# Kernel tuning notes

Hardware: AMD Instinct MI355X
Metric: run time of the kernel (lower is better)

The kernel has to match this reference:

```python
import jax, jax.numpy as jnp
import numpy as np
import itertools

WS = (4, 4, 4, 2, 2)          # window size per dim
SS = (2, 2, 2, 1, 1)          # shift size per dim
B, D, H, W, U, V, C = 1, 16, 16, 8, 8, 8, 128
HEADS = 4
HD = C // HEADS
N = WS[0] * WS[1] * WS[2] * WS[3] * WS[4]   # 256 tokens per window


def _partition(x):
    # (b, D,H,W,U,V, c) -> (b*nW, N, c)
    b, c = x.shape[0], x.shape[-1]
    x = x.reshape(b, D // WS[0], WS[0], H // WS[1], WS[1], W // WS[2], WS[2],
                  U // WS[3], WS[3], V // WS[4], WS[4], c)
    x = x.transpose(0, 1, 3, 5, 7, 9, 2, 4, 6, 8, 10, 11)
    return x.reshape(-1, N, c)


def _reverse(win, b):
    # (b*nW, N, c) -> (b, D,H,W,U,V, c)
    c = win.shape[-1]
    x = win.reshape(b, D // WS[0], H // WS[1], W // WS[2], U // WS[3], V // WS[4],
                    WS[0], WS[1], WS[2], WS[3], WS[4], c)
    x = x.transpose(0, 1, 6, 2, 7, 3, 8, 4, 9, 5, 10, 11)
    return x.reshape(b, D, H, W, U, V, c)


def _ln(x, w, b, eps=1e-5):
    mu = jnp.mean(x, -1, keepdims=True)
    xc = x - mu
    var = jnp.mean(xc * xc, -1, keepdims=True)
    return xc * jax.lax.rsqrt(var + eps) * w + b


def _compute_mask():
    # 5D generalization of Swin's compute_mask: region labels then pairwise diff
    img = np.zeros((1, D, H, W, U, V, 1), np.float32)
    slcs = [[slice(0, -w), slice(-w, -s), slice(-s, None)] for w, s in zip(WS, SS)]
    cnt = 0
    for idx in itertools.product(*slcs):
        img[(slice(None),) + idx] = cnt
        cnt += 1
    mw = np.asarray(_partition(jnp.asarray(img))).squeeze(-1)  # (nW, N)
    diff = mw[:, None, :] - mw[:, :, None]
    return jnp.asarray(np.where(diff != 0, -1e9, 0.0).astype(np.float32))


def setup_inputs() -> dict:
    key = jax.random.key(0)
    ks = jax.random.split(key, 6)
    s = 0.02
    return {
        "x": jax.random.normal(ks[0], (B, D, H, W, U, V, C), jnp.float32),
        "mask": _compute_mask(),  # (512, 256, 256)
        "qkv_w": jax.random.normal(ks[1], (3 * C, C), jnp.float32) * s,
        "qkv_b": jnp.zeros((3 * C,), jnp.float32),
        "proj_w": jax.random.normal(ks[2], (C, C), jnp.float32) * s,
        "proj_b": jnp.zeros((C,), jnp.float32),
        "norm1_w": jnp.ones((C,), jnp.float32),
        "norm1_b": jnp.zeros((C,), jnp.float32),
        "norm2_w": jnp.ones((C,), jnp.float32),
        "norm2_b": jnp.zeros((C,), jnp.float32),
        "fc1_w": jax.random.normal(ks[3], (4 * C, C), jnp.float32) * s,
        "fc1_b": jnp.zeros((4 * C,), jnp.float32),
        "fc2_w": jax.random.normal(ks[4], (C, 4 * C), jnp.float32) * s,
        "fc2_b": jnp.zeros((C,), jnp.float32),
    }


def reference(x, mask, qkv_w, qkv_b, proj_w, proj_b, norm1_w, norm1_b,
              norm2_w, norm2_b, fc1_w, fc1_b, fc2_w, fc2_b):
    shortcut = x
    h = _ln(x, norm1_w, norm1_b)
    # cyclic shift
    h = jnp.roll(h, shift=tuple(-s for s in SS), axis=(1, 2, 3, 4, 5))
    win = _partition(h)                                # (nW, N, C)
    nw = win.shape[0]
    qkv = win @ qkv_w.T + qkv_b                        # (nW, N, 3C)
    qkv = qkv.reshape(nw, N, 3, HEADS, HD).transpose(2, 0, 3, 1, 4)
    q, k, v = qkv[0] * (HD ** -0.5), qkv[1], qkv[2]    # (nW, heads, N, hd)
    logits = jnp.einsum('bhnc,bhmc->bhnm', q, k) + mask[:, None]
    attn = jax.nn.softmax(logits, axis=-1)
    o = jnp.einsum('bhnm,bhmc->bhnc', attn, v)
    o = o.transpose(0, 2, 1, 3).reshape(nw, N, C)
    o = o @ proj_w.T + proj_b
    h = _reverse(o, B)
    # reverse cyclic shift
    h = jnp.roll(h, shift=SS, axis=(1, 2, 3, 4, 5))
    x = shortcut + h
    m = _ln(x, norm2_w, norm2_b)
    m = jax.nn.gelu(m @ fc1_w.T + fc1_b, approximate=False)
    m = m @ fc2_w.T + fc2_b
    return x + m
```

## Files before the change

kernel.cpp:

```cpp
#include <hip/hip_runtime.h>
#include <math.h>

typedef short bf16x8 __attribute__((ext_vector_type(8)));
typedef float f32x4 __attribute__((ext_vector_type(4)));
typedef unsigned short ushort_t;
typedef unsigned int uint_t;

__device__ __forceinline__ float bf2f(ushort_t h) { return __uint_as_float(((uint_t)h) << 16); }
__device__ __forceinline__ ushort_t f2bf(float f) {
    uint_t u = __float_as_uint(f);
    u += 0x7fffu + ((u >> 16) & 1u);
    return (ushort_t)(u >> 16);
}
__device__ __forceinline__ float bflo(uint_t u) { return __uint_as_float(u << 16); }
__device__ __forceinline__ float bfhi(uint_t u) { return __uint_as_float(u & 0xffff0000u); }

__device__ __forceinline__ bool probe_f32(const void* ones) {
    return ((const ushort_t*)ones)[0] == 0;
}

__device__ __forceinline__ void load8f(const void* p, size_t idx, bool f32, float* o) {
    if (f32) {
        const float4* q = (const float4*)((const float*)p + idx);
        float4 a = q[0], b = q[1];
        o[0] = a.x; o[1] = a.y; o[2] = a.z; o[3] = a.w;
        o[4] = b.x; o[5] = b.y; o[6] = b.z; o[7] = b.w;
    } else {
        uint4 u = *(const uint4*)((const ushort_t*)p + idx);
        o[0] = bflo(u.x); o[1] = bfhi(u.x); o[2] = bflo(u.y); o[3] = bfhi(u.y);
        o[4] = bflo(u.z); o[5] = bfhi(u.z); o[6] = bflo(u.w); o[7] = bfhi(u.w);
    }
}

__device__ __forceinline__ float load1(const void* p, size_t i, bool f32) {
    return f32 ? ((const float*)p)[i] : bf2f(((const ushort_t*)p)[i]);
}
__device__ __forceinline__ void store1(void* p, size_t i, bool f32, float v) {
    if (f32) ((float*)p)[i] = v;
    else ((ushort_t*)p)[i] = f2bf(v);
}

__device__ __forceinline__ float gelu_f(float x) {
    float ax = fabsf(x) * 0.70710678118654752f;
    float t = __builtin_amdgcn_rcpf(1.f + 0.3275911f * ax);
    float p = t * (0.254829592f +
              t * (-0.284496736f +
              t * (1.421413741f +
              t * (-1.453152027f +
              t * 1.061405429f))));
    float e = __expf(-ax * ax);
    float erfv = 1.f - p * e;
    float phi = 0.5f * (1.f + copysignf(erfv, x));
    return x * phi;
}

__device__ __forceinline__ void token_g(int t, int g[5]) {
    int n = t & 255, w = t >> 8;
    int wv = w & 3, wu = (w >> 2) & 3, ww = (w >> 4) & 1, wh = (w >> 5) & 3, wd = (w >> 7) & 3;
    int iv = n & 1, iu = (n >> 1) & 1, iw = (n >> 2) & 3, ih = (n >> 4) & 3, id = (n >> 6) & 3;
    g[0] = wd * 4 + id;
    g[1] = wh * 4 + ih;
    g[2] = ww * 4 + iw;
    g[3] = wu * 2 + iu;
    g[4] = wv * 2 + iv;
}

__device__ __forceinline__ int token_shiftpix(int t) {
    int g[5];
    token_g(t, g);
    int d = (g[0] + 2) & 15, h = (g[1] + 2) & 15, w = (g[2] + 2) & 7;
    int u = (g[3] + 1) & 7, v = (g[4] + 1) & 7;
    return ((((d * 16 + h) * 8 + w) * 8 + u) * 8 + v);
}

__device__ __forceinline__ int token_label(int t) {
    int g[5];
    token_g(t, g);
    int r0 = g[0] < 12 ? 0 : (g[0] < 14 ? 1 : 2);
    int r1 = g[1] < 12 ? 0 : (g[1] < 14 ? 1 : 2);
    int r2 = g[2] < 4 ? 0 : (g[2] < 6 ? 1 : 2);
    int r3 = g[3] < 6 ? 0 : (g[3] < 7 ? 1 : 2);
    int r4 = g[4] < 6 ? 0 : (g[4] < 7 ? 1 : 2);
    return (((r0 * 3 + r1) * 3 + r2) * 3 + r3) * 3 + r4;
}

#define MFMA16(a, b, c) __builtin_amdgcn_mfma_f32_16x16x32_bf16(a, b, c, 0, 0, 0)

#define QW_N 49152
#define PW_N 16384
#define W1_N 65536
#define W2_N 65536

__global__ __launch_bounds__(256) void k_prep(const void* __restrict__ qw,
                                              const void* __restrict__ pw,
                                              const void* __restrict__ w1,
                                              const void* __restrict__ w2,
                                              const void* __restrict__ probe,
                                              ushort_t* __restrict__ out) {
    const bool f32 = probe_f32(probe);
    size_t e = ((size_t)blockIdx.x * 256 + threadIdx.x) * 8;
    float v[8];
    size_t dst;
    if (e < QW_N) {
        load8f(qw, e, f32, v);
        dst = e;
    } else if (e < QW_N + PW_N) {
        load8f(pw, e - QW_N, f32, v);
        dst = e;
    } else if (e < QW_N + PW_N + W1_N) {
        size_t off = e - (QW_N + PW_N);
        load8f(w1, off, f32, v);
        int n = (int)(off >> 7), k = (int)(off & 127);
        int chunk = ((n >> 4) * 4 + (k >> 5)) * 64 + ((k >> 3) & 3) * 16 + (n & 15);
        dst = (size_t)(QW_N + PW_N) + (size_t)chunk * 8;
    } else {
        size_t off = e - (QW_N + PW_N + W1_N);
        load8f(w2, off, f32, v);
        int n = (int)(off >> 9), k = (int)(off & 511);
        int chunk = ((n >> 4) * 16 + (k >> 5)) * 64 + ((k >> 3) & 3) * 16 + (n & 15);
        dst = (size_t)(QW_N + PW_N + W1_N) + (size_t)chunk * 8;
    }
    union { uint4 q; ushort_t u[8]; } pk;
#pragma unroll
    for (int j = 0; j < 8; j++) pk.u[j] = f2bf(v[j]);
    *reinterpret_cast<uint4*>(out + dst) = pk.q;
}

__global__ __launch_bounds__(256) void k_qkv(const void* __restrict__ x,
                                             const void* __restrict__ n1w,
                                             const void* __restrict__ n1b,
                                             const ushort_t* __restrict__ qwb,
                                             const void* __restrict__ qb,
                                             ushort_t* __restrict__ qT,
                                             ushort_t* __restrict__ kT,
                                             ushort_t* __restrict__ vF) {
    __shared__ __align__(16) ushort_t sA[128][136];
    __shared__ __align__(16) ushort_t sB[128][136];
    const bool f32 = probe_f32(n1w);
    const int tid = threadIdx.x;
    const int ct = blockIdx.x;
    const int rt = blockIdx.y;

    {
        int i = tid >> 1, half = tid & 1;
        int t = rt * 128 + i;
        int pix = token_shiftpix(t);
        float v[64];
        float s1 = 0.f, s2 = 0.f;
#pragma unroll
        for (int j = 0; j < 8; j++) {
            load8f(x, (size_t)pix * 128 + half * 64 + j * 8, f32, &v[j * 8]);
#pragma unroll
            for (int e = 0; e < 8; e++) { float f = v[j * 8 + e]; s1 += f; s2 += f * f; }
        }
        s1 += __shfl_xor(s1, 1);
        s2 += __shfl_xor(s2, 1);
        float mean = s1 * (1.f / 128.f);
        float var = s2 * (1.f / 128.f) - mean * mean;
        float rstd = rsqrtf(fmaxf(var, 0.f) + 1e-5f);
#pragma unroll
        for (int j = 0; j < 64; j++) {
            int c = half * 64 + j;
            float nv = (v[j] - mean) * rstd * load1(n1w, c, f32) + load1(n1b, c, f32);
            sA[i][c] = f2bf(nv);
        }
    }
    {
        int i = tid >> 1, half = tid & 1;
        const uint4* wr = (const uint4*)(qwb + (size_t)(ct * 128 + i) * 128 + half * 64);
#pragma unroll
        for (int j = 0; j < 8; j++)
            *reinterpret_cast<uint4*>(&sB[i][half * 64 + j * 8]) = wr[j];
    }
    __syncthreads();

    const int lane = tid & 63, wvid = tid >> 6;
    const int quad = lane >> 4, l16 = lane & 15;
    const int mbase = (wvid >> 1) * 64, nbase = (wvid & 1) * 64;
    f32x4 acc[4][4];
#pragma unroll
    for (int a = 0; a < 4; a++)
#pragma unroll
        for (int b = 0; b < 4; b++) acc[a][b] = (f32x4){0.f, 0.f, 0.f, 0.f};

#pragma unroll
    for (int k0 = 0; k0 < 128; k0 += 32) {
        bf16x8 af[4], bg[4];
#pragma unroll
        for (int mi = 0; mi < 4; mi++)
            af[mi] = *reinterpret_cast<const bf16x8*>(&sA[mbase + mi * 16 + l16][k0 + quad * 8]);
#pragma unroll
        for (int ni = 0; ni < 4; ni++)
            bg[ni] = *reinterpret_cast<const bf16x8*>(&sB[nbase + ni * 16 + l16][k0 + quad * 8]);
#pragma unroll
        for (int mi = 0; mi < 4; mi++)
#pragma unroll
            for (int ni = 0; ni < 4; ni++) acc[mi][ni] = MFMA16(af[mi], bg[ni], acc[mi][ni]);
    }
    const int wbase4 = (rt >> 1) * 4;
    const int nadd = (rt & 1) * 128;
#pragma unroll
    for (int ni = 0; ni < 4; ni++) {
        int col = nbase + ni * 16 + l16;
        float bias = load1(qb, ct * 128 + col, f32);
        int h = col >> 5, d = col & 31;
        size_t whbase = (size_t)(wbase4 + h) * 8192;
#pragma unroll
        for (int mi = 0; mi < 4; mi++) {
#pragma unroll
            for (int r = 0; r < 4; r++) {
                int row = mbase + mi * 16 + quad * 4 + r;
                int n = nadd + row;
                float val = acc[mi][ni][r] + bias;
                if (ct == 0) {
                    qT[whbase + (size_t)n * 32 + d] = f2bf(val);
                } else if (ct == 1) {
                    kT[whbase + (size_t)n * 32 + d] = f2bf(val);
                } else {
                    size_t idx = whbase + (size_t)(n >> 5) * 1024 + (size_t)(d >> 4) * 512 +
                                 (size_t)((n >> 3) & 3) * 128 + (size_t)(d & 15) * 8 + (n & 7);
                    vF[idx] = f2bf(val);
                }
            }
        }
    }
}

__global__ __launch_bounds__(256) void k_attn(const ushort_t* __restrict__ qT,
                                              const ushort_t* __restrict__ kT,
                                              const ushort_t* __restrict__ vF,
                                              ushort_t* __restrict__ o) {
    __shared__ __align__(16) ushort_t sS[64][264];
    __shared__ unsigned char sLab[256];
    const int tid = threadIdx.x;
    const int rb = blockIdx.x, hh = blockIdx.y, w = blockIdx.z;
    const size_t whbase = (size_t)(w * 4 + hh) * 8192;

    sLab[tid] = (unsigned char)token_label(w * 256 + tid);
    __syncthreads();

    const int lane = tid & 63, wvid = tid >> 6, quad = lane >> 4, l16 = lane & 15;
    const int r0 = wvid * 16;

    bf16x8 aq = *reinterpret_cast<const bf16x8*>(
        qT + whbase + (size_t)(rb * 64 + r0 + l16) * 32 + quad * 8);

    f32x4 s[16];
    int myLab[4];
#pragma unroll
    for (int r = 0; r < 4; r++) myLab[r] = sLab[rb * 64 + r0 + quad * 4 + r];
#pragma unroll
    for (int ni = 0; ni < 16; ni++) {
        bf16x8 bk = *reinterpret_cast<const bf16x8*>(
            kT + whbase + (size_t)(ni * 16 + l16) * 32 + quad * 8);
        f32x4 c = (f32x4){0.f, 0.f, 0.f, 0.f};
        c = MFMA16(aq, bk, c);
        int klab = sLab[ni * 16 + l16];
#pragma unroll
        for (int r = 0; r < 4; r++)
            s[ni][r] = (klab == myLab[r]) ? c[r] * 0.17677669529663687f : -1.0e30f;
    }
    float mx[4], sm[4], inv[4];
#pragma unroll
    for (int r = 0; r < 4; r++) {
        float m2 = s[0][r];
#pragma unroll
        for (int ni = 1; ni < 16; ni++) m2 = fmaxf(m2, s[ni][r]);
        m2 = fmaxf(m2, __shfl_xor(m2, 1));
        m2 = fmaxf(m2, __shfl_xor(m2, 2));
        m2 = fmaxf(m2, __shfl_xor(m2, 4));
        m2 = fmaxf(m2, __shfl_xor(m2, 8));
        mx[r] = m2;
    }
#pragma unroll
    for (int r = 0; r < 4; r++) sm[r] = 0.f;
#pragma unroll
    for (int ni = 0; ni < 16; ni++) {
#pragma unroll
        for (int r = 0; r < 4; r++) {
            float p = __expf(s[ni][r] - mx[r]);
            s[ni][r] = p;
            sm[r] += p;
        }
    }
#pragma unroll
    for (int r = 0; r < 4; r++) {
        float t2 = sm[r];
        t2 += __shfl_xor(t2, 1);
        t2 += __shfl_xor(t2, 2);
        t2 += __shfl_xor(t2, 4);
        t2 += __shfl_xor(t2, 8);
        inv[r] = 1.f / t2;
    }
#pragma unroll
    for (int ni = 0; ni < 16; ni++) {
#pragma unroll
        for (int r = 0; r < 4; r++)
            sS[r0 + quad * 4 + r][ni * 16 + l16] = f2bf(s[ni][r]);
    }
    __syncthreads();

    f32x4 oacc[2];
    oacc[0] = (f32x4){0.f, 0.f, 0.f, 0.f};
    oacc[1] = (f32x4){0.f, 0.f, 0.f, 0.f};
#pragma unroll
    for (int kt = 0; kt < 8; kt++) {
        bf16x8 ap = *reinterpret_cast<const bf16x8*>(&sS[r0 + l16][kt * 32 + quad * 8]);
#pragma unroll
        for (int t2 = 0; t2 < 2; t2++) {
            bf16x8 bv = *reinterpret_cast<const bf16x8*>(
                vF + whbase + (size_t)((kt * 2 + t2) * 64 + lane) * 8);
            oacc[t2] = MFMA16(ap, bv, oacc[t2]);
        }
    }
#pragma unroll
    for (int t2 = 0; t2 < 2; t2++) {
#pragma unroll
        for (int r = 0; r < 4; r++) {
            int row = r0 + quad * 4 + r;
            int tok = w * 256 + rb * 64 + row;
            o[(size_t)tok * 128 + hh * 32 + t2 * 16 + l16] = f2bf(oacc[t2][r] * inv[r]);
        }
    }
}

__global__ __launch_bounds__(256) void k_proj(const ushort_t* __restrict__ o,
                                              const ushort_t* __restrict__ pwb,
                                              const void* __restrict__ pb,
                                              const void* __restrict__ x,
                                              const void* __restrict__ n1w,
                                              float* __restrict__ x2) {
    __shared__ __align__(16) ushort_t sA[128][136];
    __shared__ __align__(16) ushort_t sB[128][136];
    __shared__ int sPix[128];
    const bool f32 = probe_f32(n1w);
    const int tid = threadIdx.x;
    const int rt = blockIdx.x;

    if (tid < 128) sPix[tid] = token_shiftpix(rt * 128 + tid);
    {
        int i = tid >> 1, half = tid & 1;
        const uint4* src = (const uint4*)(o + (size_t)(rt * 128 + i) * 128 + half * 64);
        const uint4* wsrc = (const uint4*)(pwb + (size_t)i * 128 + half * 64);
#pragma unroll
        for (int j = 0; j < 8; j++) {
            *reinterpret_cast<uint4*>(&sA[i][half * 64 + j * 8]) = src[j];
            *reinterpret_cast<uint4*>(&sB[i][half * 64 + j * 8]) = wsrc[j];
        }
    }
    __syncthreads();

    const int lane = tid & 63, wvid = tid >> 6;
    const int quad = lane >> 4, l16 = lane & 15;
    const int mbase = (wvid >> 1) * 64, nbase = (wvid & 1) * 64;
    f32x4 acc[4][4];
#pragma unroll
    for (int a = 0; a < 4; a++)
#pragma unroll
        for (int b = 0; b < 4; b++) acc[a][b] = (f32x4){0.f, 0.f, 0.f, 0.f};

#pragma unroll
    for (int k0 = 0; k0 < 128; k0 += 32) {
        bf16x8 af[4], bg[4];
#pragma unroll
        for (int mi = 0; mi < 4; mi++)
            af[mi] = *reinterpret_cast<const bf16x8*>(&sA[mbase + mi * 16 + l16][k0 + quad * 8]);
#pragma unroll
        for (int ni = 0; ni < 4; ni++)
            bg[ni] = *reinterpret_cast<const bf16x8*>(&sB[nbase + ni * 16 + l16][k0 + quad * 8]);
#pragma unroll
        for (int mi = 0; mi < 4; mi++)
#pragma unroll
            for (int ni = 0; ni < 4; ni++) acc[mi][ni] = MFMA16(af[mi], bg[ni], acc[mi][ni]);
    }
#pragma unroll
    for (int ni = 0; ni < 4; ni++) {
        int col = nbase + ni * 16 + l16;
        float bias = load1(pb, col, f32);
#pragma unroll
        for (int mi = 0; mi < 4; mi++) {
#pragma unroll
            for (int r = 0; r < 4; r++) {
                int row = mbase + mi * 16 + quad * 4 + r;
                int pix = sPix[row];
                size_t idx = (size_t)pix * 128 + col;
                x2[idx] = acc[mi][ni][r] + bias + load1(x, idx, f32);
            }
        }
    }
}

__global__ __launch_bounds__(256) void k_mlp(const float* __restrict__ x2,
                                             const void* __restrict__ n2w,
                                             const void* __restrict__ n2b,
                                             const ushort_t* __restrict__ w1f,
                                             const void* __restrict__ b1,
                                             const ushort_t* __restrict__ w2f,
                                             const void* __restrict__ b2,
                                             void* __restrict__ out) {
    __shared__ __align__(16) ushort_t sH[32][516];
    ushort_t (*sM)[136] = reinterpret_cast<ushort_t (*)[136]>(&sH[0][0]);
    const bool f32 = probe_f32(n2w);
    const int tid = threadIdx.x;
    const int t0 = blockIdx.x * 32;

    {
        int i = tid >> 3, oct = tid & 7;
        const float* row = x2 + (size_t)(t0 + i) * 128 + oct * 16;
        float v[16];
        float s1 = 0.f, s2 = 0.f;
#pragma unroll
        for (int j = 0; j < 4; j++) {
            float4 f = ((const float4*)row)[j];
            v[j * 4 + 0] = f.x; v[j * 4 + 1] = f.y; v[j * 4 + 2] = f.z; v[j * 4 + 3] = f.w;
            s1 += f.x + f.y + f.z + f.w;
            s2 += f.x * f.x + f.y * f.y + f.z * f.z + f.w * f.w;
        }
        s1 += __shfl_xor(s1, 1); s2 += __shfl_xor(s2, 1);
        s1 += __shfl_xor(s1, 2); s2 += __shfl_xor(s2, 2);
        s1 += __shfl_xor(s1, 4); s2 += __shfl_xor(s2, 4);
        float mean = s1 * (1.f / 128.f);
        float rstd = rsqrtf(fmaxf(s2 * (1.f / 128.f) - mean * mean, 0.f) + 1e-5f);
#pragma unroll
        for (int j = 0; j < 16; j++) {
            int c = oct * 16 + j;
            sM[i][c] = f2bf((v[j] - mean) * rstd * load1(n2w, c, f32) + load1(n2b, c, f32));
        }
    }
    __syncthreads();

    const int lane = tid & 63, wvid = tid >> 6, quad = lane >> 4, l16 = lane & 15;

    bf16x8 af[2][4];
#pragma unroll
    for (int mi = 0; mi < 2; mi++)
#pragma unroll
        for (int k4 = 0; k4 < 4; k4++)
            af[mi][k4] = *reinterpret_cast<const bf16x8*>(&sM[mi * 16 + l16][k4 * 32 + quad * 8]);
    __syncthreads();

    {
        const int cb = wvid * 128;
        bf16x8 wf[4], wn[4];
#pragma unroll
        for (int k4 = 0; k4 < 4; k4++)
            wf[k4] = *reinterpret_cast<const bf16x8*>(
                w1f + (size_t)(((wvid * 8) * 4 + k4) * 64 + lane) * 8);
#pragma unroll
        for (int ni = 0; ni < 8; ni++) {
            if (ni < 7) {
#pragma unroll
                for (int k4 = 0; k4 < 4; k4++)
                    wn[k4] = *reinterpret_cast<const bf16x8*>(
                        w1f + (size_t)(((wvid * 8 + ni + 1) * 4 + k4) * 64 + lane) * 8);
            }
            f32x4 a0 = (f32x4){0.f, 0.f, 0.f, 0.f};
            f32x4 a1 = (f32x4){0.f, 0.f, 0.f, 0.f};
#pragma unroll
            for (int k4 = 0; k4 < 4; k4++) {
                a0 = MFMA16(af[0][k4], wf[k4], a0);
                a1 = MFMA16(af[1][k4], wf[k4], a1);
            }
            int col = cb + ni * 16 + l16;
            float bias = load1(b1, col, f32);
#pragma unroll
            for (int r = 0; r < 4; r++) {
                sH[quad * 4 + r][col] = f2bf(gelu_f(a0[r] + bias));
                sH[16 + quad * 4 + r][col] = f2bf(gelu_f(a1[r] + bias));
            }
#pragma unroll
            for (int k4 = 0; k4 < 4; k4++) wf[k4] = wn[k4];
        }
    }
    __syncthreads();
    {
        const int cb = wvid * 32;
        float res[2][2][4];
#pragma unroll
        for (int mi = 0; mi < 2; mi++)
#pragma unroll
            for (int ni = 0; ni < 2; ni++)
#pragma unroll
                for (int r = 0; r < 4; r++)
                    res[mi][ni][r] = x2[(size_t)(t0 + mi * 16 + quad * 4 + r) * 128 + cb + ni * 16 + l16];
        f32x4 acc[2][2];
#pragma unroll
        for (int mi = 0; mi < 2; mi++)
#pragma unroll
            for (int ni = 0; ni < 2; ni++) acc[mi][ni] = (f32x4){0.f, 0.f, 0.f, 0.f};
        bf16x8 wf[2], wn[2];
#pragma unroll
        for (int ni = 0; ni < 2; ni++)
            wf[ni] = *reinterpret_cast<const bf16x8*>(
                w2f + (size_t)(((wvid * 2 + ni) * 16) * 64 + lane) * 8);
#pragma unroll
        for (int k0 = 0; k0 < 16; k0++) {
            if (k0 < 15) {
#pragma unroll
                for (int ni = 0; ni < 2; ni++)
                    wn[ni] = *reinterpret_cast<const bf16x8*>(
                        w2f + (size_t)(((wvid * 2 + ni) * 16 + k0 + 1) * 64 + lane) * 8);
            }
            bf16x8 a0 = *reinterpret_cast<const bf16x8*>(&sH[l16][k0 * 32 + quad * 8]);
            bf16x8 a1 = *reinterpret_cast<const bf16x8*>(&sH[16 + l16][k0 * 32 + quad * 8]);
            acc[0][0] = MFMA16(a0, wf[0], acc[0][0]);
            acc[1][0] = MFMA16(a1, wf[0], acc[1][0]);
            acc[0][1] = MFMA16(a0, wf[1], acc[0][1]);
            acc[1][1] = MFMA16(a1, wf[1], acc[1][1]);
            wf[0] = wn[0];
            wf[1] = wn[1];
        }
#pragma unroll
        for (int ni = 0; ni < 2; ni++) {
            int col = cb + ni * 16 + l16;
            float bias = load1(b2, col, f32);
#pragma unroll
            for (int mi = 0; mi < 2; mi++) {
#pragma unroll
                for (int r = 0; r < 4; r++) {
                    int row = mi * 16 + quad * 4 + r;
                    size_t idx = (size_t)(t0 + row) * 128 + col;
                    store1(out, idx, f32, acc[mi][ni][r] + bias + res[mi][ni][r]);
                }
            }
        }
    }
}

extern "C" void kernel_launch(void* const* d_in, const int* in_sizes, int n_in,
                              void* d_out, int out_size, void* d_ws, size_t ws_size,
                              hipStream_t stream) {
    (void)in_sizes; (void)n_in; (void)out_size; (void)ws_size;
    const void* x   = d_in[0];
    const void* qw  = d_in[2];
    const void* qb  = d_in[3];
    const void* pw  = d_in[4];
    const void* pb  = d_in[5];
    const void* n1w = d_in[6];
    const void* n1b = d_in[7];
    const void* n2w = d_in[8];
    const void* n2b = d_in[9];
    const void* w1  = d_in[10];
    const void* b1  = d_in[11];
    const void* w2  = d_in[12];
    const void* b2  = d_in[13];

    ushort_t* qT  = (ushort_t*)d_ws;
    ushort_t* kT  = (ushort_t*)((char*)d_ws + 33554432);
    ushort_t* vF  = (ushort_t*)((char*)d_ws + 67108864);
    ushort_t* ob  = (ushort_t*)((char*)d_ws + 100663296);
    float* x2     = (float*)d_ws;
    ushort_t* wts = (ushort_t*)((char*)d_ws + 134217728);
    ushort_t* qwb = wts;
    ushort_t* pwb = wts + QW_N;
    ushort_t* w1f = wts + QW_N + PW_N;
    ushort_t* w2f = wts + QW_N + PW_N + W1_N;

    hipLaunchKernelGGL(k_prep, dim3(96), dim3(256), 0, stream, qw, pw, w1, w2, n1w, wts);
    hipLaunchKernelGGL(k_qkv, dim3(3, 1024), dim3(256), 0, stream, x, n1w, n1b, qwb, qb, qT, kT, vF);
    hipLaunchKernelGGL(k_attn, dim3(4, 4, 512), dim3(256), 0, stream, qT, kT, vF, ob);
    hipLaunchKernelGGL(k_proj, dim3(1024), dim3(256), 0, stream, ob, pwb, pb, x, n1w, x2);
    hipLaunchKernelGGL(k_mlp, dim3(4096), dim3(256), 0, stream, x2, n2w, n2b, w1f, b1, w2f, b2, d_out);
}
```

Before: 560.6 us.

## Merge QKV column tiles per block and read MFMA-fragment weights from global

The QKV kernel now handles all three Q/K/V column tiles in one block, looping over them, so the LayerNorm of x is done once per row tile instead of three times. The prep kernel reorders the qkv and proj weights into an MFMA fragment-major layout, so the B operand is loaded straight from global/L2 with coalesced 16-byte loads and no shared-memory staging. Halving shared memory plus launch_bounds(256,4) is meant to raise occupancy. The trade-off is that weight reads now depend on cache hits from global memory, and each block does more serial work over a grid three times smaller.

```diff
diff --git a/kernel.cpp b/kernel.cpp
--- a/kernel.cpp
+++ b/kernel.cpp
@@ -103,10 +103,15 @@
     size_t dst;
     if (e < QW_N) {
         load8f(qw, e, f32, v);
-        dst = e;
+        int n = (int)(e >> 7), k = (int)(e & 127);
+        int chunk = ((n >> 4) * 4 + (k >> 5)) * 64 + ((k >> 3) & 3) * 16 + (n & 15);
+        dst = (size_t)chunk * 8;
     } else if (e < QW_N + PW_N) {
-        load8f(pw, e - QW_N, f32, v);
-        dst = e;
+        size_t off = e - QW_N;
+        load8f(pw, off, f32, v);
+        int n = (int)(off >> 7), k = (int)(off & 127);
+        int chunk = ((n >> 4) * 4 + (k >> 5)) * 64 + ((k >> 3) & 3) * 16 + (n & 15);
+        dst = (size_t)QW_N + (size_t)chunk * 8;
     } else if (e < QW_N + PW_N + W1_N) {
         size_t off = e - (QW_N + PW_N);
         load8f(w1, off, f32, v);
@@ -126,20 +131,18 @@
     *reinterpret_cast<uint4*>(out + dst) = pk.q;
 }
 
-__global__ __launch_bounds__(256) void k_qkv(const void* __restrict__ x,
-                                             const void* __restrict__ n1w,
-                                             const void* __restrict__ n1b,
-                                             const ushort_t* __restrict__ qwb,
-                                             const void* __restrict__ qb,
-                                             ushort_t* __restrict__ qT,
-                                             ushort_t* __restrict__ kT,
-                                             ushort_t* __restrict__ vF) {
+__global__ __launch_bounds__(256, 4) void k_qkv(const void* __restrict__ x,
+                                                const void* __restrict__ n1w,
+                                                const void* __restrict__ n1b,
+                                                const ushort_t* __restrict__ qwF,
+                                                const void* __restrict__ qb,
+                                                ushort_t* __restrict__ qT,
+                                                ushort_t* __restrict__ kT,
+                                                ushort_t* __restrict__ vF) {
     __shared__ __align__(16) ushort_t sA[128][136];
-    __shared__ __align__(16) ushort_t sB[128][136];
     const bool f32 = probe_f32(n1w);
     const int tid = threadIdx.x;
-    const int ct = blockIdx.x;
-    const int rt = blockIdx.y;
+    const int rt = blockIdx.x;
 
     {
         int i = tid >> 1, half = tid & 1;
@@ -159,67 +162,70 @@
         float var = s2 * (1.f / 128.f) - mean * mean;
         float rstd = rsqrtf(fmaxf(var, 0.f) + 1e-5f);
 #pragma unroll
-        for (int j = 0; j < 64; j++) {
-            int c = half * 64 + j;
-            float nv = (v[j] - mean) * rstd * load1(n1w, c, f32) + load1(n1b, c, f32);
-            sA[i][c] = f2bf(nv);
-        }
-    }
-    {
-        int i = tid >> 1, half = tid & 1;
-        const uint4* wr = (const uint4*)(qwb + (size_t)(ct * 128 + i) * 128 + half * 64);
-#pragma unroll
-        for (int j = 0; j < 8; j++)
-            *reinterpret_cast<uint4*>(&sB[i][half * 64 + j * 8]) = wr[j];
-    }
-    __syncthreads();
-
-    const int lane = tid & 63, wvid = tid >> 6;
-    const int quad = lane >> 4, l16 = lane & 15;
+        for (int j = 0; j < 8; j++) {
+            float wv[8], bv[8];
+            load8f(n1w, half * 64 + j * 8, f32, wv);
+            load8f(n1b, half * 64 + j * 8, f32, bv);
+            union { uint4 q; ushort_t u[8]; } pk;
+#pragma unroll
+            for (int e = 0; e < 8; e++)
+                pk.u[e] = f2bf((v[j * 8 + e] - mean) * rstd * wv[e] + bv[e]);
+            *reinterpret_cast<uint4*>(&sA[i][half * 64 + j * 8]) = pk.q;
+        }
+    }
+    __syncthreads();
+
+    const int lane = tid & 63, wvid = tid >> 6, quad = lane >> 4, l16 = lane & 15;
     const int mbase = (wvid >> 1) * 64, nbase = (wvid & 1) * 64;
-    f32x4 acc[4][4];
-#pragma unroll
-    for (int a = 0; a < 4; a++)
-#pragma unroll
-        for (int b = 0; b < 4; b++) acc[a][b] = (f32x4){0.f, 0.f, 0.f, 0.f};
-
-#pragma unroll
-    for (int k0 = 0; k0 < 128; k0 += 32) {
-        bf16x8 af[4], bg[4];
-#pragma unroll
-        for (int mi = 0; mi < 4; mi++)
-            af[mi] = *reinterpret_cast<const bf16x8*>(&sA[mbase + mi * 16 + l16][k0 + quad * 8]);
-#pragma unroll
-        for (int ni = 0; ni < 4; ni++)
-            bg[ni] = *reinterpret_cast<const bf16x8*>(&sB[nbase + ni * 16 + l16][k0 + quad * 8]);
-#pragma unroll
-        for (int mi = 0; mi < 4; mi++)
-#pragma unroll
-            for (int ni = 0; ni < 4; ni++) acc[mi][ni] = MFMA16(af[mi], bg[ni], acc[mi][ni]);
-    }
+    const int tnb = (wvid & 1) * 4;
     const int wbase4 = (rt >> 1) * 4;
     const int nadd = (rt & 1) * 128;
-#pragma unroll
-    for (int ni = 0; ni < 4; ni++) {
-        int col = nbase + ni * 16 + l16;
-        float bias = load1(qb, ct * 128 + col, f32);
-        int h = col >> 5, d = col & 31;
-        size_t whbase = (size_t)(wbase4 + h) * 8192;
-#pragma unroll
-        for (int mi = 0; mi < 4; mi++) {
-#pragma unroll
-            for (int r = 0; r < 4; r++) {
-                int row = mbase + mi * 16 + quad * 4 + r;
-                int n = nadd + row;
-                float val = acc[mi][ni][r] + bias;
-                if (ct == 0) {
-                    qT[whbase + (size_t)n * 32 + d] = f2bf(val);
-                } else if (ct == 1) {
-                    kT[whbase + (size_t)n * 32 + d] = f2bf(val);
-                } else {
-                    size_t idx = whbase + (size_t)(n >> 5) * 1024 + (size_t)(d >> 4) * 512 +
-                                 (size_t)((n >> 3) & 3) * 128 + (size_t)(d & 15) * 8 + (n & 7);
-                    vF[idx] = f2bf(val);
+
+#pragma unroll 1
+    for (int ct = 0; ct < 3; ct++) {
+        f32x4 acc[4][4];
+#pragma unroll
+        for (int a = 0; a < 4; a++)
+#pragma unroll
+            for (int b = 0; b < 4; b++) acc[a][b] = (f32x4){0.f, 0.f, 0.f, 0.f};
+
+#pragma unroll
+        for (int k4 = 0; k4 < 4; k4++) {
+            bf16x8 af[4], bg[4];
+#pragma unroll
+            for (int mi = 0; mi < 4; mi++)
+                af[mi] = *reinterpret_cast<const bf16x8*>(&sA[mbase + mi * 16 + l16][k4 * 32 + quad * 8]);
+#pragma unroll
+            for (int ni = 0; ni < 4; ni++)
+                bg[ni] = *reinterpret_cast<const bf16x8*>(
+                    qwF + (size_t)(((ct * 8 + tnb + ni) * 4 + k4) * 64 + lane) * 8);
+#pragma unroll
+            for (int mi = 0; mi < 4; mi++)
+#pragma unroll
+                for (int ni = 0; ni < 4; ni++) acc[mi][ni] = MFMA16(af[mi], bg[ni], acc[mi][ni]);
+        }
+#pragma unroll
+        for (int ni = 0; ni < 4; ni++) {
+            int col = nbase + ni * 16 + l16;
+            float bias = load1(qb, ct * 128 + col, f32);
+            int h = col >> 5, d = col & 31;
+            size_t whbase = (size_t)(wbase4 + h) * 8192;
+#pragma unroll
+            for (int mi = 0; mi < 4; mi++) {
+#pragma unroll
+                for (int r = 0; r < 4; r++) {
+                    int row = mbase + mi * 16 + quad * 4 + r;
+                    int n = nadd + row;
+                    float val = acc[mi][ni][r] + bias;
+                    if (ct == 0) {
+                        qT[whbase + (size_t)n * 32 + d] = f2bf(val);
+                    } else if (ct == 1) {
+                        kT[whbase + (size_t)n * 32 + d] = f2bf(val);
+                    } else {
+                        size_t idx = whbase + (size_t)(n >> 5) * 1024 + (size_t)(d >> 4) * 512 +
+                                     (size_t)((n >> 3) & 3) * 128 + (size_t)(d & 15) * 8 + (n & 7);
+                        vF[idx] = f2bf(val);
+                    }
                 }
             }
         }
@@ -324,14 +330,13 @@
     }
 }
 
-__global__ __launch_bounds__(256) void k_proj(const ushort_t* __restrict__ o,
-                                              const ushort_t* __restrict__ pwb,
-                                              const void* __restrict__ pb,
-                                              const void* __restrict__ x,
-                                              const void* __restrict__ n1w,
-                                              float* __restrict__ x2) {
+__global__ __launch_bounds__(256, 4) void k_proj(const ushort_t* __restrict__ o,
+                                                 const ushort_t* __restrict__ pwF,
+                                                 const void* __restrict__ pb,
+                                                 const void* __restrict__ x,
+                                                 const void* __restrict__ n1w,
+                                                 float* __restrict__ x2) {
     __shared__ __align__(16) ushort_t sA[128][136];
-    __shared__ __align__(16) ushort_t sB[128][136];
     __shared__ int sPix[128];
     const bool f32 = probe_f32(n1w);
     const int tid = threadIdx.x;
@@ -341,18 +346,16 @@
     {
         int i = tid >> 1, half = tid & 1;
         const uint4* src = (const uint4*)(o + (size_t)(rt * 128 + i) * 128 + half * 64);
-        const uint4* wsrc = (const uint4*)(pwb + (size_t)i * 128 + half * 64);
-#pragma unroll
-        for (int j = 0; j < 8; j++) {
+#pragma unroll
+        for (int j = 0; j < 8; j++)
             *reinterpret_cast<uint4*>(&sA[i][half * 64 + j * 8]) = src[j];
-            *reinterpret_cast<uint4*>(&sB[i][half * 64 + j * 8]) = wsrc[j];
-        }
     }
     __syncthreads();
 
     const int lane = tid & 63, wvid = tid >> 6;
     const int quad = lane >> 4, l16 = lane & 15;
     const int mbase = (wvid >> 1) * 64, nbase = (wvid & 1) * 64;
+    const int tnb = (wvid & 1) * 4;
     f32x4 acc[4][4];
 #pragma unroll
     for (int a = 0; a < 4; a++)
@@ -360,14 +363,15 @@
         for (int b = 0; b < 4; b++) acc[a][b] = (f32x4){0.f, 0.f, 0.f, 0.f};
 
 #pragma unroll
-    for (int k0 = 0; k0 < 128; k0 += 32) {
+    for (int k4 = 0; k4 < 4; k4++) {
         bf16x8 af[4], bg[4];
 #pragma unroll
         for (int mi = 0; mi < 4; mi++)
-            af[mi] = *reinterpret_cast<const bf16x8*>(&sA[mbase + mi * 16 + l16][k0 + quad * 8]);
+            af[mi] = *reinterpret_cast<const bf16x8*>(&sA[mbase + mi * 16 + l16][k4 * 32 + quad * 8]);
 #pragma unroll
         for (int ni = 0; ni < 4; ni++)
-            bg[ni] = *reinterpret_cast<const bf16x8*>(&sB[nbase + ni * 16 + l16][k0 + quad * 8]);
+            bg[ni] = *reinterpret_cast<const bf16x8*>(
+                pwF + (size_t)(((tnb + ni) * 4 + k4) * 64 + lane) * 8);
 #pragma unroll
         for (int mi = 0; mi < 4; mi++)
 #pragma unroll
@@ -551,14 +555,14 @@
     ushort_t* ob  = (ushort_t*)((char*)d_ws + 100663296);
     float* x2     = (float*)d_ws;
     ushort_t* wts = (ushort_t*)((char*)d_ws + 134217728);
-    ushort_t* qwb = wts;
-    ushort_t* pwb = wts + QW_N;
+    ushort_t* qwF = wts;
+    ushort_t* pwF = wts + QW_N;
     ushort_t* w1f = wts + QW_N + PW_N;
     ushort_t* w2f = wts + QW_N + PW_N + W1_N;
 
     hipLaunchKernelGGL(k_prep, dim3(96), dim3(256), 0, stream, qw, pw, w1, w2, n1w, wts);
-    hipLaunchKernelGGL(k_qkv, dim3(3, 1024), dim3(256), 0, stream, x, n1w, n1b, qwb, qb, qT, kT, vF);
+    hipLaunchKernelGGL(k_qkv, dim3(1024), dim3(256), 0, stream, x, n1w, n1b, qwF, qb, qT, kT, vF);
     hipLaunchKernelGGL(k_attn, dim3(4, 4, 512), dim3(256), 0, stream, qT, kT, vF, ob);
-    hipLaunchKernelGGL(k_proj, dim3(1024), dim3(256), 0, stream, ob, pwb, pb, x, n1w, x2);
+    hipLaunchKernelGGL(k_proj, dim3(1024), dim3(256), 0, stream, ob, pwF, pb, x, n1w, x2);
     hipLaunchKernelGGL(k_mlp, dim3(4096), dim3(256), 0, stream, x2, n2w, n2b, w1f, b1, w2f, b2, d_out);
 }
```

Measured after the change: 696.7 us. +24.3%, slower.
